# Performance work log

Measured on AMD Instinct MI355X. Metric: run time of the kernel, lower is better.

Reference implementation:

```python
import jax, jax.numpy as jnp
import numpy as np

EMB = 1024
HEAD = 128

def setup_inputs() -> dict:
    key = jax.random.key(0)
    ks = jax.random.split(key, 7)
    B, S = 4, 4096
    x = jax.random.normal(ks[0], (B, S, EMB), dtype=jnp.float32)
    s_in = 1.0 / np.sqrt(EMB)
    Wq = jax.random.uniform(ks[1], (EMB, HEAD), jnp.float32, -s_in, s_in)
    bq = jax.random.uniform(ks[2], (HEAD,), jnp.float32, -s_in, s_in)
    Wk = jax.random.uniform(ks[3], (EMB, HEAD), jnp.float32, -s_in, s_in)
    bk = jax.random.uniform(ks[4], (HEAD,), jnp.float32, -s_in, s_in)
    Wv = jax.random.uniform(ks[5], (EMB, HEAD), jnp.float32, -s_in, s_in)
    bv = jax.random.uniform(ks[6], (HEAD,), jnp.float32, -s_in, s_in)
    return {"decoder_sequence": x, "Wq": Wq, "bq": bq, "Wk": Wk, "bk": bk, "Wv": Wv, "bv": bv}

def reference(decoder_sequence, Wq, bq, Wk, bk, Wv, bv):
    # QKV projections: [B,S,E] @ [E,H] -> [B,S,H]
    Q = decoder_sequence @ Wq + bq
    K = decoder_sequence @ Wk + bk
    V = decoder_sequence @ Wv + bv
    S = decoder_sequence.shape[1]
    scale = 1.0 / jnp.sqrt(jnp.asarray(HEAD, Q.dtype))
    # scores [B,S,S]
    A = jnp.einsum('bid,bjd->bij', Q, K) * scale
    causal = jnp.tril(jnp.ones((S, S), dtype=bool))  # keep lower-triangular incl. diag
    A = jnp.where(causal, A, -jnp.inf)
    A = jax.nn.softmax(A, axis=-1)
    return jnp.einsum('bij,bjd->bid', A, V)
```

## Files before the change

kernel.cpp:

```cpp
#include <hip/hip_runtime.h>
#include <hip/hip_bf16.h>
#include <math.h>

#define S_LEN 4096
#define EMB   1024
#define HEAD  128

typedef short bf16x8 __attribute__((ext_vector_type(8)));
typedef short s16x4  __attribute__((ext_vector_type(4)));
typedef float f32x4  __attribute__((ext_vector_type(4)));

static __device__ __forceinline__ short f2bf(float x){
  unsigned u = __builtin_bit_cast(unsigned, x);
  u += 0x7fffu + ((u >> 16) & 1u);
  return (short)(u >> 16);
}
static __device__ __forceinline__ float bf2f(short s){
  unsigned u = ((unsigned)(unsigned short)s) << 16;
  return __builtin_bit_cast(float, u);
}
static __device__ __forceinline__ f32x4 mfma16(bf16x8 a, bf16x8 b, f32x4 c){
  return __builtin_amdgcn_mfma_f32_16x16x32_bf16(a, b, c, 0, 0, 0);
}
static __device__ __forceinline__ void gload16(const void* g, void* l){
  __builtin_amdgcn_global_load_lds((const __attribute__((address_space(1))) unsigned*)g,
                                   (__attribute__((address_space(3))) unsigned*)l, 16, 0, 0);
}

__global__ void prep_w(const float* __restrict__ Wq, const float* __restrict__ bq,
                       const float* __restrict__ Wk, const float* __restrict__ bk,
                       const float* __restrict__ Wv, const float* __restrict__ bv,
                       short* __restrict__ WT, float* __restrict__ bias){
  const float QS = 0.08838834764831845f * 1.4426950408889634f;
  int idx = blockIdx.x * 256 + threadIdx.x;
  int nc  = idx >> 10;
  int k   = idx & 1023;
  int mat = nc >> 7;
  int n   = nc & 127;
  const float* W = (mat == 0) ? Wq : (mat == 1) ? Wk : Wv;
  float s = (mat == 0) ? QS : 1.0f;
  WT[idx] = f2bf(W[k * HEAD + n] * s);
  if (idx < 384){
    int m2 = idx >> 7, n2 = idx & 127;
    const float* bsrc = (m2 == 0) ? bq : (m2 == 1) ? bk : bv;
    float s2 = (m2 == 0) ? QS : 1.0f;
    bias[idx] = bsrc[n2] * s2;
  }
}

__global__ __launch_bounds__(1024) void qkv_proj(const float* __restrict__ x,
    const short* __restrict__ WT, const float* __restrict__ bias,
    short* __restrict__ Qo, short* __restrict__ Ko, short* __restrict__ VTo){
  __shared__ __align__(16) short Sm[2][32768];

  const int tid = threadIdx.x;
  const int wave = tid >> 6, lane = tid & 63, lr = lane & 15, hg = lane >> 4;
  const int wrg = wave >> 3, cg = wave & 7, fbase = cg * 3;
  const int row0 = blockIdx.x * 64;

  const f32x4 zero = {0.f, 0.f, 0.f, 0.f};
  f32x4 acc[2][3];
  #pragma unroll
  for (int rf = 0; rf < 2; ++rf)
    #pragma unroll
    for (int f = 0; f < 3; ++f) acc[rf][f] = zero;

#define WL(buf) (&Sm[buf][0])
#define XL(buf) ((float*)&Sm[buf][24576])

#define QKV_STAGE(buf, k0)                                                         \
  {                                                                                \
    _Pragma("unroll")                                                              \
    for (int s = 0; s < 3; ++s){                                                   \
      int slot = s * 16 + wave;                                                    \
      int ff = slot >> 1, ks = slot & 1;                                           \
      gload16(WT + (size_t)(ff * 16 + lr) * 1024 + (k0) + ks * 32 + hg * 8,        \
              WL(buf) + slot * 512);                                               \
    }                                                                              \
    {                                                                              \
      int rr = wave * 4 + hg;                                                      \
      int cs = lr ^ (rr & 15);                                                     \
      gload16(x + (size_t)(row0 + rr) * 1024 + (k0) + cs * 4,                      \
              XL(buf) + wave * 256);                                               \
    }                                                                              \
  }

  QKV_STAGE(0, 0)

  int cur = 0;
  for (int t = 0; t < 16; ++t){
    if (t < 15){
      QKV_STAGE(cur ^ 1, (t + 1) * 64)
      asm volatile("s_waitcnt vmcnt(4)" ::: "memory");
    } else {
      asm volatile("s_waitcnt vmcnt(0)" ::: "memory");
    }
    __builtin_amdgcn_s_barrier();
    asm volatile("" ::: "memory");

    bf16x8 a[2][2];
    #pragma unroll
    for (int rf = 0; rf < 2; ++rf){
      const int xr = wrg * 32 + rf * 16 + lr;
      #pragma unroll
      for (int ks = 0; ks < 2; ++ks){
        int s0 = ks * 8 + hg * 2;
        f32x4 xa = *(const f32x4*)&XL(cur)[xr * 64 + ((s0 ^ lr) << 2)];
        f32x4 xb = *(const f32x4*)&XL(cur)[xr * 64 + (((s0 + 1) ^ lr) << 2)];
        a[rf][ks][0] = f2bf(xa[0]); a[rf][ks][1] = f2bf(xa[1]);
        a[rf][ks][2] = f2bf(xa[2]); a[rf][ks][3] = f2bf(xa[3]);
        a[rf][ks][4] = f2bf(xb[0]); a[rf][ks][5] = f2bf(xb[1]);
        a[rf][ks][6] = f2bf(xb[2]); a[rf][ks][7] = f2bf(xb[3]);
      }
    }
    __builtin_amdgcn_s_setprio(1);
    #pragma unroll
    for (int fi = 0; fi < 3; ++fi){
      #pragma unroll
      for (int ks = 0; ks < 2; ++ks){
        bf16x8 bfr = *(const bf16x8*)&WL(cur)[((fbase + fi) * 2 + ks) * 512 + lane * 8];
        acc[0][fi] = mfma16(a[0][ks], bfr, acc[0][fi]);
        acc[1][fi] = mfma16(a[1][ks], bfr, acc[1][fi]);
      }
    }
    __builtin_amdgcn_s_setprio(0);
    asm volatile("" ::: "memory");
    __builtin_amdgcn_s_barrier();
    cur ^= 1;
  }

  short* Vb = &Sm[0][0];
  #pragma unroll
  for (int rf = 0; rf < 2; ++rf){
    #pragma unroll
    for (int fi = 0; fi < 3; ++fi){
      int f = fbase + fi;
      float bb = bias[f * 16 + lr];
      int rloc = wrg * 32 + rf * 16 + hg * 4;
      if (f < 16){
        short* dst = (f < 8) ? Qo : Ko;
        int col = (f & 7) * 16 + lr;
        #pragma unroll
        for (int r = 0; r < 4; ++r)
          dst[(size_t)(row0 + rloc + r) * HEAD + col] = f2bf(acc[rf][fi][r] + bb);
      } else {
        int vcol = (f - 16) * 16 + lr;
        #pragma unroll
        for (int r = 0; r < 4; ++r)
          Vb[vcol * 72 + rloc + r] = f2bf(acc[rf][fi][r] + bb);
      }
    }
  }
  __syncthreads();
  {
    int vcol = tid >> 3, sq = tid & 7;
    bf16x8 v = *(const bf16x8*)&Vb[vcol * 72 + sq * 8];
    int bb2 = row0 >> 12, ss = row0 & 4095;
    *(bf16x8*)(VTo + ((size_t)(bb2 * HEAD + vcol)) * S_LEN + ss + sq * 8) = v;
  }
}

#define PPS 36

__global__ __launch_bounds__(128, 2) void attn(const short* __restrict__ Q,
    const short* __restrict__ K, const short* __restrict__ VT,
    short* __restrict__ Opart, float* __restrict__ Dn){
  __shared__ __align__(16) short Kl[2][4096];
  __shared__ __align__(16) short Vl[2][4096];
  __shared__ __align__(16) short Pl[2][2][16 * PPS];

  const int tid = threadIdx.x;
  const int wave = tid >> 6, lane = tid & 63, lr = lane & 15, hg = lane >> 4;
  const int b = blockIdx.x;
  const int i = blockIdx.y;

  int t, c;
  if (i < 232){
    c = 0;
    #pragma unroll
    for (int j = 1; j < 8; ++j) if (i >= j * (61 - 4 * j)) c = j;
    t = 8 * c + 7 + (i - c * (61 - 4 * c));
  } else {
    int p = i - 232;
    t = p + p / 7;
    c = t >> 3;
  }

  const int qt0  = t * 64;
  const int kvlo = c << 9;
  const int kvhi = min(kvlo + 512, qt0 + 64);
  const int ns   = (kvhi - kvlo) >> 5;

  const short* Qg = Q  + ((size_t)b * S_LEN + qt0 + wave * 32) * HEAD;
  const short* Kg = K  + (size_t)b * S_LEN * HEAD;
  const short* Vg = VT + (size_t)b * HEAD * S_LEN;

  bf16x8 qf[2][4];
  #pragma unroll
  for (int qs = 0; qs < 2; ++qs)
    #pragma unroll
    for (int sl = 0; sl < 4; ++sl)
      qf[qs][sl] = *(const bf16x8*)(Qg + (size_t)(qs * 16 + lr) * HEAD + sl * 32 + hg * 8);

#define ATTN_STAGE(buf, j0)                                                        \
  {                                                                                \
    if (wave == 0){                                                                \
      _Pragma("unroll")                                                            \
      for (int s = 0; s < 8; ++s)                                                  \
        gload16(Kg + (size_t)((j0) + (s >> 2) * 16 + lr) * HEAD + (s & 3) * 32 + hg * 8, \
                &Kl[buf][s * 512]);                                                \
    } else {                                                                       \
      _Pragma("unroll")                                                            \
      for (int s = 0; s < 8; ++s)                                                  \
        gload16(Vg + (size_t)(s * 16 + lr) * S_LEN + (j0) + hg * 8,                \
                &Vl[buf][s * 512]);                                                \
    }                                                                              \
  }

  ATTN_STAGE(0, kvlo)

  const f32x4 zero = {0.f, 0.f, 0.f, 0.f};
  f32x4 acc[8][2];
  #pragma unroll
  for (int f = 0; f < 8; ++f){ acc[f][0] = zero; acc[f][1] = zero; }
  float den[2] = {0.f, 0.f};

  int cur = 0;
  for (int st = 0; st < ns; ++st){
    const int j0 = kvlo + st * 32;
    if (st + 1 < ns){
      ATTN_STAGE(cur ^ 1, j0 + 32)
      asm volatile("s_waitcnt vmcnt(8)" ::: "memory");
    } else {
      asm volatile("s_waitcnt vmcnt(0)" ::: "memory");
    }
    __builtin_amdgcn_s_barrier();
    asm volatile("" ::: "memory");

    f32x4 sc[2][2];
    __builtin_amdgcn_s_setprio(1);
    #pragma unroll
    for (int kvs = 0; kvs < 2; ++kvs){
      sc[kvs][0] = zero; sc[kvs][1] = zero;
      #pragma unroll
      for (int sl = 0; sl < 4; ++sl){
        bf16x8 kf = *(const bf16x8*)&Kl[cur][(kvs * 4 + sl) * 512 + lane * 8];
        sc[kvs][0] = mfma16(kf, qf[0][sl], sc[kvs][0]);
        sc[kvs][1] = mfma16(kf, qf[1][sl], sc[kvs][1]);
      }
    }
    __builtin_amdgcn_s_setprio(0);

    if (j0 + 31 > qt0 + wave * 32){
      #pragma unroll
      for (int qs = 0; qs < 2; ++qs){
        int qr0 = qt0 + wave * 32 + qs * 16;
        #pragma unroll
        for (int kvs = 0; kvs < 2; ++kvs){
          int kv0 = j0 + kvs * 16 + hg * 4;
          #pragma unroll
          for (int r = 0; r < 4; ++r)
            if (kv0 + r > qr0 + lr) sc[kvs][qs][r] = -INFINITY;
        }
      }
    }

    s16x4 pb[2][2];
    #pragma unroll
    for (int qs = 0; qs < 2; ++qs){
      #pragma unroll
      for (int r = 0; r < 4; ++r){
        float p0 = __builtin_exp2f(sc[0][qs][r]);
        float p1 = __builtin_exp2f(sc[1][qs][r]);
        den[qs] += p0 + p1;
        pb[qs][0][r] = f2bf(p0); pb[qs][1][r] = f2bf(p1);
      }
    }

    #pragma unroll
    for (int qs = 0; qs < 2; ++qs){
      short* Pw = &Pl[wave][qs][0];
      *(s16x4*)(&Pw[lr * PPS + hg * 4])      = pb[qs][0];
      *(s16x4*)(&Pw[lr * PPS + 16 + hg * 4]) = pb[qs][1];
    }

    bf16x8 vf[8];
    #pragma unroll
    for (int f = 0; f < 8; ++f)
      vf[f] = *(const bf16x8*)&Vl[cur][f * 512 + lane * 8];

    bf16x8 pf[2];
    #pragma unroll
    for (int qs = 0; qs < 2; ++qs)
      pf[qs] = *(const bf16x8*)(&Pl[wave][qs][lr * PPS + hg * 8]);

    __builtin_amdgcn_s_setprio(1);
    #pragma unroll
    for (int f = 0; f < 8; ++f){
      acc[f][0] = mfma16(vf[f], pf[0], acc[f][0]);
      acc[f][1] = mfma16(vf[f], pf[1], acc[f][1]);
    }
    __builtin_amdgcn_s_setprio(0);

    asm volatile("" ::: "memory");
    __builtin_amdgcn_s_barrier();
    cur ^= 1;
  }

  #pragma unroll
  for (int qs = 0; qs < 2; ++qs){
    den[qs] += __shfl_xor(den[qs], 16);
    den[qs] += __shfl_xor(den[qs], 32);
  }

  const int pidx = b * 288 + i;
  short* Op = Opart + (size_t)pidx * 8192;
  #pragma unroll
  for (int qs = 0; qs < 2; ++qs){
    const int rowblk = wave * 2 + qs;
    #pragma unroll
    for (int f = 0; f < 8; ++f){
      s16x4 ov;
      #pragma unroll
      for (int r = 0; r < 4; ++r) ov[r] = f2bf(acc[f][qs][r]);
      *(s16x4*)(Op + (rowblk * 16 + lr) * 128 + f * 16 + hg * 4) = ov;
    }
    if (hg == 0)
      Dn[pidx * 64 + rowblk * 16 + lr] = den[qs];
  }
}

__global__ __launch_bounds__(512) void combine(const short* __restrict__ Opart,
    const float* __restrict__ Dn, float* __restrict__ out){
  const int t = blockIdx.x, b = blockIdx.y;
  const int row = threadIdx.x >> 3;
  const int cgp = threadIdx.x & 7;
  const int nc = (t >> 3) + 1;
  const int nheavy = (t + 1) >> 3;

  float L = 0.f;
  float o[16];
  #pragma unroll
  for (int e = 0; e < 16; ++e) o[e] = 0.f;
  for (int cc = 0; cc < nc; ++cc){
    int ii = (cc < nheavy) ? cc * (61 - 4 * cc) + t - (8 * cc + 7)
                           : 232 + t - (t >> 3);
    int id = b * 288 + ii;
    L += Dn[id * 64 + row];
    const short* op = Opart + (size_t)id * 8192 + row * 128 + cgp * 16;
    bf16x8 v0 = *(const bf16x8*)(op);
    bf16x8 v1 = *(const bf16x8*)(op + 8);
    #pragma unroll
    for (int e = 0; e < 8; ++e){
      o[e]     += bf2f(v0[e]);
      o[8 + e] += bf2f(v1[e]);
    }
  }
  float inv = 1.f / L;
  float* dst = out + ((size_t)b * S_LEN + t * 64 + row) * HEAD + cgp * 16;
  #pragma unroll
  for (int e4 = 0; e4 < 4; ++e4){
    float4 w4 = { o[e4*4]*inv, o[e4*4+1]*inv, o[e4*4+2]*inv, o[e4*4+3]*inv };
    *(float4*)(dst + e4 * 4) = w4;
  }
}

extern "C" void kernel_launch(void* const* d_in, const int* in_sizes, int n_in,
                              void* d_out, int out_size, void* d_ws, size_t ws_size,
                              hipStream_t stream){
  const float* x  = (const float*)d_in[0];
  const float* Wq = (const float*)d_in[1];
  const float* bq = (const float*)d_in[2];
  const float* Wk = (const float*)d_in[3];
  const float* bk = (const float*)d_in[4];
  const float* Wv = (const float*)d_in[5];
  const float* bv = (const float*)d_in[6];
  float* out = (float*)d_out;

  char* ws = (char*)d_ws;
  short* WT    = (short*)(ws);
  float* bias  = (float*)(ws + 786432);
  short* Qb    = (short*)(ws + (1u << 20));
  short* Kb    = (short*)(ws + (1u << 20) + 4194304u);
  short* VTb   = (short*)(ws + (1u << 20) + 8388608u);
  short* Opart = (short*)(ws + 13631488u);
  float* Dn    = (float*)(ws + 32505856u);

  prep_w<<<1536, 256, 0, stream>>>(Wq, bq, Wk, bk, Wv, bv, WT, bias);
  qkv_proj<<<256, 1024, 0, stream>>>(x, WT, bias, Qb, Kb, VTb);
  attn<<<dim3(4, 288), 128, 0, stream>>>(Qb, Kb, VTb, Opart, Dn);
  combine<<<dim3(64, 4), 512, 0, stream>>>(Opart, Dn, out);
}
```

Measured before the change: 100.7 us.

## Enlarge attention query tile to 128 rows with four waves sharing K/V stages

The attention kernel now runs four waves per block covering 128 query rows instead of two waves covering 64. Each staged 32-key K/V tile is therefore reused by twice as many query rows, which halves the K/V global and L2 traffic per query. The K and V loads are split evenly across all four waves, and the block-to-(query tile, key chunk) mapping plus the combine indexing are rebuilt for the 128-row tiles. The cost is half as many blocks and coarser work units, which may hurt load balance and occupancy.

```diff
diff --git a/kernel.cpp b/kernel.cpp
--- a/kernel.cpp
+++ b/kernel.cpp
@@ -162,34 +162,34 @@
 
 #define PPS 36
 
-__global__ __launch_bounds__(128, 2) void attn(const short* __restrict__ Q,
+__global__ __launch_bounds__(256) void attn(const short* __restrict__ Q,
     const short* __restrict__ K, const short* __restrict__ VT,
     short* __restrict__ Opart, float* __restrict__ Dn){
   __shared__ __align__(16) short Kl[2][4096];
   __shared__ __align__(16) short Vl[2][4096];
-  __shared__ __align__(16) short Pl[2][2][16 * PPS];
+  __shared__ __align__(16) short Pl[4][2][16 * PPS];
 
   const int tid = threadIdx.x;
   const int wave = tid >> 6, lane = tid & 63, lr = lane & 15, hg = lane >> 4;
   const int b = blockIdx.x;
   const int i = blockIdx.y;
 
-  int t, c;
-  if (i < 232){
-    c = 0;
-    #pragma unroll
-    for (int j = 1; j < 8; ++j) if (i >= j * (61 - 4 * j)) c = j;
-    t = 8 * c + 7 + (i - c * (61 - 4 * c));
-  } else {
-    int p = i - 232;
-    t = p + p / 7;
-    c = t >> 3;
-  }
-
-  const int qt0  = t * 64;
+  int t, c, ns;
+  if (i < 120){
+    int acc2 = 0; t = 0; c = 0;
+    #pragma unroll
+    for (int tt = 0; tt < 32; ++tt){
+      int nf = (tt >> 2) + ((tt & 3) == 3);
+      if (i >= acc2 && i < acc2 + nf){ t = tt; c = i - acc2; }
+      acc2 += nf;
+    }
+    ns = 16;
+  } else if (i < 128){ int k = i - 120; t = 4 * k + 2; c = k; ns = 12; }
+  else if (i < 136)  { int k = i - 128; t = 4 * k + 1; c = k; ns = 8; }
+  else               { int k = i - 136; t = 4 * k;     c = k; ns = 4; }
+
+  const int qt0  = t * 128;
   const int kvlo = c << 9;
-  const int kvhi = min(kvlo + 512, qt0 + 64);
-  const int ns   = (kvhi - kvlo) >> 5;
 
   const short* Qg = Q  + ((size_t)b * S_LEN + qt0 + wave * 32) * HEAD;
   const short* Kg = K  + (size_t)b * S_LEN * HEAD;
@@ -204,16 +204,17 @@
 
 #define ATTN_STAGE(buf, j0)                                                        \
   {                                                                                \
-    if (wave == 0){                                                                \
-      _Pragma("unroll")                                                            \
-      for (int s = 0; s < 8; ++s)                                                  \
-        gload16(Kg + (size_t)((j0) + (s >> 2) * 16 + lr) * HEAD + (s & 3) * 32 + hg * 8, \
-                &Kl[buf][s * 512]);                                                \
-    } else {                                                                       \
-      _Pragma("unroll")                                                            \
-      for (int s = 0; s < 8; ++s)                                                  \
-        gload16(Vg + (size_t)(s * 16 + lr) * S_LEN + (j0) + hg * 8,                \
-                &Vl[buf][s * 512]);                                                \
+    _Pragma("unroll")                                                              \
+    for (int q = 0; q < 2; ++q){                                                   \
+      int s = wave * 2 + q;                                                        \
+      gload16(Kg + (size_t)((j0) + (s >> 2) * 16 + lr) * HEAD + (s & 3) * 32 + hg * 8, \
+              &Kl[buf][s * 512]);                                                  \
+    }                                                                              \
+    _Pragma("unroll")                                                              \
+    for (int q = 0; q < 2; ++q){                                                   \
+      int s = wave * 2 + q;                                                        \
+      gload16(Vg + (size_t)(s * 16 + lr) * S_LEN + (j0) + hg * 8,                  \
+              &Vl[buf][s * 512]);                                                  \
     }                                                                              \
   }
 
@@ -230,7 +231,7 @@
     const int j0 = kvlo + st * 32;
     if (st + 1 < ns){
       ATTN_STAGE(cur ^ 1, j0 + 32)
-      asm volatile("s_waitcnt vmcnt(8)" ::: "memory");
+      asm volatile("s_waitcnt vmcnt(4)" ::: "memory");
     } else {
       asm volatile("s_waitcnt vmcnt(0)" ::: "memory");
     }
@@ -283,12 +284,10 @@
       *(s16x4*)(&Pw[lr * PPS + hg * 4])      = pb[qs][0];
       *(s16x4*)(&Pw[lr * PPS + 16 + hg * 4]) = pb[qs][1];
     }
-
     bf16x8 vf[8];
     #pragma unroll
     for (int f = 0; f < 8; ++f)
       vf[f] = *(const bf16x8*)&Vl[cur][f * 512 + lane * 8];
-
     bf16x8 pf[2];
     #pragma unroll
     for (int qs = 0; qs < 2; ++qs)
@@ -313,8 +312,8 @@
     den[qs] += __shfl_xor(den[qs], 32);
   }
 
-  const int pidx = b * 288 + i;
-  short* Op = Opart + (size_t)pidx * 8192;
+  const int pidx = b * 144 + i;
+  short* Op = Opart + (size_t)pidx * 16384;
   #pragma unroll
   for (int qs = 0; qs < 2; ++qs){
     const int rowblk = wave * 2 + qs;
@@ -326,28 +325,32 @@
       *(s16x4*)(Op + (rowblk * 16 + lr) * 128 + f * 16 + hg * 4) = ov;
     }
     if (hg == 0)
-      Dn[pidx * 64 + rowblk * 16 + lr] = den[qs];
+      Dn[pidx * 128 + rowblk * 16 + lr] = den[qs];
   }
 }
 
 __global__ __launch_bounds__(512) void combine(const short* __restrict__ Opart,
     const float* __restrict__ Dn, float* __restrict__ out){
-  const int t = blockIdx.x, b = blockIdx.y;
+  const int bx = blockIdx.x, b = blockIdx.y;
+  const int t = bx >> 1, sub = bx & 1;
   const int row = threadIdx.x >> 3;
   const int cgp = threadIdx.x & 7;
-  const int nc = (t >> 3) + 1;
-  const int nheavy = (t + 1) >> 3;
+  const int rI = sub * 64 + row;
+  const int a = t >> 2, bb = t & 3;
+  const int Ffull = a * (2 * a + bb - 1);
+  const int nfull = a + (bb == 3);
+  const int nc = a + 1;
+  const int ipart = (bb == 2) ? 120 + a : (bb == 1) ? 128 + a : 136 + a;
 
   float L = 0.f;
   float o[16];
   #pragma unroll
   for (int e = 0; e < 16; ++e) o[e] = 0.f;
   for (int cc = 0; cc < nc; ++cc){
-    int ii = (cc < nheavy) ? cc * (61 - 4 * cc) + t - (8 * cc + 7)
-                           : 232 + t - (t >> 3);
-    int id = b * 288 + ii;
-    L += Dn[id * 64 + row];
-    const short* op = Opart + (size_t)id * 8192 + row * 128 + cgp * 16;
+    int ii = (cc < nfull) ? Ffull + cc : ipart;
+    int id = b * 144 + ii;
+    L += Dn[id * 128 + rI];
+    const short* op = Opart + (size_t)id * 16384 + rI * 128 + cgp * 16;
     bf16x8 v0 = *(const bf16x8*)(op);
     bf16x8 v1 = *(const bf16x8*)(op + 8);
     #pragma unroll
@@ -357,7 +360,7 @@
     }
   }
   float inv = 1.f / L;
-  float* dst = out + ((size_t)b * S_LEN + t * 64 + row) * HEAD + cgp * 16;
+  float* dst = out + ((size_t)b * S_LEN + t * 128 + rI) * HEAD + cgp * 16;
   #pragma unroll
   for (int e4 = 0; e4 < 4; ++e4){
     float4 w4 = { o[e4*4]*inv, o[e4*4+1]*inv, o[e4*4+2]*inv, o[e4*4+3]*inv };
@@ -388,6 +391,6 @@
 
   prep_w<<<1536, 256, 0, stream>>>(Wq, bq, Wk, bk, Wv, bv, WT, bias);
   qkv_proj<<<256, 1024, 0, stream>>>(x, WT, bias, Qb, Kb, VTb);
-  attn<<<dim3(4, 288), 128, 0, stream>>>(Qb, Kb, VTb, Opart, Dn);
+  attn<<<dim3(4, 144), 256, 0, stream>>>(Qb, Kb, VTb, Opart, Dn);
   combine<<<dim3(64, 4), 512, 0, stream>>>(Opart, Dn, out);
 }
```

Measured after the change: 96.35 us. 1.04x faster.
